# Kernel tuning notes

Measured on AMD Instinct MI355X. Metric: run time of the kernel, lower is better.

The kernel has to match this reference:

```python
import jax, jax.numpy as jnp
import numpy as np

C = 256

def setup_inputs() -> dict:
    key = jax.random.key(0)
    ks = jax.random.split(key, 9)
    B, H, W = 32, 32, 32
    s = C ** -0.5  # init scale for weights
    inputs = jax.random.normal(ks[0], (B, H, W, C), jnp.float32)
    Wq = jax.random.normal(ks[1], (C, C), jnp.float32) * s
    Wk = jax.random.normal(ks[2], (C, C), jnp.float32) * s
    Wv = jax.random.normal(ks[3], (C, C), jnp.float32) * s
    Wo = jax.random.normal(ks[4], (C, C), jnp.float32) * s
    bq = jnp.zeros((C,), jnp.float32)
    bk = jnp.zeros((C,), jnp.float32)
    bv = jnp.zeros((C,), jnp.float32)
    bo = jnp.zeros((C,), jnp.float32)
    return {"inputs": inputs, "Wq": Wq, "bq": bq, "Wk": Wk, "bk": bk,
            "Wv": Wv, "bv": bv, "Wo": Wo, "bo": bo}

def reference(inputs, Wq, bq, Wk, bk, Wv, bv, Wo, bo):
    B, H, W, c = inputs.shape
    scale = jnp.float32(c) ** -0.5
    x = inputs.reshape(B, H * W, c)           # 1x1 conv == per-pixel matmul
    q = x @ Wq + bq                           # [B, HW, C]
    k = x @ Wk + bk
    v = x @ Wv + bv
    scores = jnp.einsum('bnc,bmc->bnm', q, k) * scale  # [B, HW, HW]
    attn = jax.nn.softmax(scores, axis=-1)
    attended = jnp.einsum('bnm,bmc->bnc', attn, v)     # [B, HW, C]
    out = attended @ Wo + bo
    return out.reshape(B, H, W, c)
```

## Files before the change

### kernel.cpp

```cpp
#include <hip/hip_runtime.h>
#include <hip/hip_bf16.h>

typedef __bf16 bf16;
typedef __bf16 bf16x4 __attribute__((ext_vector_type(4)));
typedef __bf16 bf16x8 __attribute__((ext_vector_type(8)));
typedef float f32x4 __attribute__((ext_vector_type(4)));

#define SM_C 0.09016994374947424f

__global__ __launch_bounds__(256) void transpose_w(
    const float* __restrict__ Wq, const float* __restrict__ Wk,
    const float* __restrict__ Wv, const float* __restrict__ Wo,
    bf16* __restrict__ Wt)
{
    __shared__ float T[32][33];
    const int bid = blockIdx.x;
    const int m = bid >> 6, tile = bid & 63;
    const int tn0 = (tile >> 3) * 32, tk0 = (tile & 7) * 32;
    const float* W = (m == 0) ? Wq : (m == 1) ? Wk : (m == 2) ? Wv : Wo;

    const int t = threadIdx.x;
    const int r = t >> 3, c4 = (t & 7) * 4;

    f32x4 v = *(const f32x4*)(W + (size_t)(tk0 + r) * 256 + tn0 + c4);
#pragma unroll
    for (int j = 0; j < 4; ++j) T[r][c4 + j] = v[j];
    __syncthreads();

    bf16x4 ov;
#pragma unroll
    for (int j = 0; j < 4; ++j) ov[j] = (bf16)T[c4 + j][r];
    *(bf16x4*)(Wt + (size_t)m * 65536 + (size_t)(tn0 + r) * 256 + tk0 + c4) = ov;
}

__global__ __launch_bounds__(256, 3) void qkv_gemm(
    const float* __restrict__ X, const bf16* __restrict__ Wt,
    const float* __restrict__ bq, const float* __restrict__ bk,
    const float* __restrict__ bv,
    bf16* __restrict__ Qo, bf16* __restrict__ Ko, bf16* __restrict__ Vto)
{
    __shared__ __align__(16) char qsmem[36864];
    bf16* const Xs  = (bf16*)qsmem;
    bf16* const Ws_ = (bf16*)(qsmem + 18432);
    bf16* const Cs  = (bf16*)qsmem;

    const int t    = threadIdx.x;
    const int lane = t & 63, wv = t >> 6;
    const int quad = lane >> 4, l16 = lane & 15;
    const int bm   = blockIdx.x;
    const int bn   = blockIdx.y;
    const int proj = bn >> 1;

    const bf16* W = Wt + (size_t)proj * 65536 + (size_t)(bn & 1) * 32768;
    const float* bias = (proj == 0) ? bq : (proj == 1) ? bk : bv;

    const int m0 = t >> 3;
    const int c0 = (t & 7) * 8;

    const f32x4 zero = {0.0f, 0.0f, 0.0f, 0.0f};
    f32x4 acc[2][8];
#pragma unroll
    for (int i = 0; i < 2; ++i)
#pragma unroll
        for (int j = 0; j < 8; ++j) acc[i][j] = zero;

    f32x4 xa[4], xb[4]; bf16x8 wp[4];
#pragma unroll
    for (int p = 0; p < 4; ++p) {
        const float* px = X + (size_t)(bm * 128 + m0 + p * 32) * 256 + c0;
        xa[p] = *(const f32x4*)px; xb[p] = *(const f32x4*)(px + 4);
        wp[p] = *(const bf16x8*)(W + (size_t)(m0 + p * 32) * 256 + c0);
    }

    for (int kt = 0; kt < 4; ++kt) {
#pragma unroll
        for (int p = 0; p < 4; ++p) {
            bf16x8 r;
#pragma unroll
            for (int j = 0; j < 4; ++j) { r[j] = (bf16)xa[p][j]; r[j + 4] = (bf16)xb[p][j]; }
            *(bf16x8*)(Xs + (m0 + p * 32) * 72 + c0) = r;
            *(bf16x8*)(Ws_ + (m0 + p * 32) * 72 + c0) = wp[p];
        }
        __syncthreads();

        if (kt < 3) {
#pragma unroll
            for (int p = 0; p < 4; ++p) {
                const float* px = X + (size_t)(bm * 128 + m0 + p * 32) * 256 + (kt + 1) * 64 + c0;
                xa[p] = *(const f32x4*)px; xb[p] = *(const f32x4*)(px + 4);
                wp[p] = *(const bf16x8*)(W + (size_t)(m0 + p * 32) * 256 + (kt + 1) * 64 + c0);
            }
        }

#pragma unroll
        for (int ks = 0; ks < 2; ++ks) {
            bf16x8 a[2], bb[8];
#pragma unroll
            for (int mt = 0; mt < 2; ++mt)
                a[mt] = *(const bf16x8*)(Xs + (wv * 32 + mt * 16 + l16) * 72 + ks * 32 + quad * 8);
#pragma unroll
            for (int nt = 0; nt < 8; ++nt)
                bb[nt] = *(const bf16x8*)(Ws_ + (nt * 16 + l16) * 72 + ks * 32 + quad * 8);
#pragma unroll
            for (int mt = 0; mt < 2; ++mt)
#pragma unroll
                for (int nt = 0; nt < 8; ++nt)
                    acc[mt][nt] = __builtin_amdgcn_mfma_f32_16x16x32_bf16(
                        a[mt], bb[nt], acc[mt][nt], 0, 0, 0);
        }
        __syncthreads();
    }

    if (proj == 2) {
#pragma unroll
        for (int nt = 0; nt < 8; ++nt) {
            int col = (bn & 1) * 128 + nt * 16 + l16;
            float bvv = bias[col];
#pragma unroll
            for (int mt = 0; mt < 2; ++mt) {
                int grow0 = bm * 128 + wv * 32 + mt * 16 + quad * 4;
                bf16x4 pk;
#pragma unroll
                for (int r = 0; r < 4; ++r) pk[r] = (bf16)(acc[mt][nt][r] + bvv);
                int b = grow0 >> 10, m = grow0 & 1023;
                *(bf16x4*)(Vto + (size_t)b * 262144 + (size_t)col * 1024 + m) = pk;
            }
        }
    } else {
        bf16* dst = (proj == 0) ? Qo : Ko;
#pragma unroll
        for (int nt = 0; nt < 8; ++nt) {
            float bvv = bias[(bn & 1) * 128 + nt * 16 + l16];
#pragma unroll
            for (int mt = 0; mt < 2; ++mt)
#pragma unroll
                for (int r = 0; r < 4; ++r)
                    Cs[(wv * 32 + mt * 16 + quad * 4 + r) * 132 + nt * 16 + l16] =
                        (bf16)(acc[mt][nt][r] + bvv);
        }
        __syncthreads();
#pragma unroll
        for (int i = 0; i < 8; ++i) {
            int chunk = i * 256 + t;
            int row = chunk >> 4, cc = chunk & 15;
            bf16x8 v = *(const bf16x8*)(Cs + row * 132 + cc * 8);
            *(bf16x8*)(dst + (size_t)(bm * 128 + row) * 256 + (bn & 1) * 128 + cc * 8) = v;
        }
    }
}

__global__ __launch_bounds__(512, 2) void flash_attn(
    const bf16* __restrict__ Qr, const bf16* __restrict__ K,
    const bf16* __restrict__ Vt, const bf16* __restrict__ Wo,
    const float* __restrict__ bo, float* __restrict__ out)
{
    __shared__ __align__(16) char smem[142336];
    bf16* const Ksp0 = (bf16*)(smem);
    bf16* const Ksp1 = (bf16*)(smem + 16896);
    bf16* const Vsp0 = (bf16*)(smem + 33792);
    bf16* const Vsp1 = (bf16*)(smem + 54272);
    bf16* const Os   = (bf16*)(smem);
    bf16* const Wos  = (bf16*)(smem + 74752);

    const int t    = threadIdx.x;
    const int lane = t & 63, wv = t >> 6;
    const int quad = lane >> 4, l16 = lane & 15;
    const int b  = blockIdx.x;
    const int qt = blockIdx.y;

    char* const Pb = smem + 74752 + wv * 1024;

    bf16x8 qf[8];
    const size_t qrow = (size_t)b * 1024 + qt * 128 + wv * 16 + l16;
#pragma unroll
    for (int ks = 0; ks < 8; ++ks)
        qf[ks] = *(const bf16x8*)(Qr + qrow * 256 + ks * 32 + quad * 8);

    const f32x4 zero = {0.0f, 0.0f, 0.0f, 0.0f};
    f32x4 o[16];
#pragma unroll
    for (int n = 0; n < 16; ++n) o[n] = zero;
    float lst[4] = {0.f, 0.f, 0.f, 0.f};

    const int kv0 = t >> 4, kc0 = (t & 15) * 8;
    const int vc0 = t >> 1, vm0 = (t & 1) * 8;

    bf16x8 kp[2], vp[2];
#pragma unroll
    for (int p = 0; p < 2; ++p) {
        kp[p] = *(const bf16x8*)(K + (size_t)(b * 1024 + kv0) * 256 + kc0 + p * 128);
        vp[p] = *(const bf16x8*)(Vt + (size_t)b * 262144 + (size_t)vc0 * 1024 + vm0 + p * 16);
    }
#pragma unroll
    for (int p = 0; p < 2; ++p) {
        *(bf16x8*)(Ksp0 + kv0 * 264 + kc0 + p * 128) = kp[p];
        *(bf16x8*)(Vsp0 + vc0 * 40 + vm0 + p * 16) = vp[p];
    }
#pragma unroll
    for (int p = 0; p < 2; ++p) {
        kp[p] = *(const bf16x8*)(K + (size_t)(b * 1024 + 32 + kv0) * 256 + kc0 + p * 128);
        vp[p] = *(const bf16x8*)(Vt + (size_t)b * 262144 + (size_t)vc0 * 1024 + 32 + vm0 + p * 16);
    }

    for (int j = 0; j < 32; ++j) {
        const bf16* Kb = (j & 1) ? Ksp1 : Ksp0;
        const bf16* Vb = (j & 1) ? Vsp1 : Vsp0;
        __syncthreads();

        f32x4 s[2];
        s[0] = zero; s[1] = zero;
#pragma unroll
        for (int ks = 0; ks < 8; ++ks) {
#pragma unroll
            for (int n = 0; n < 2; ++n) {
                bf16x8 bfr = *(const bf16x8*)(Kb + (n * 16 + l16) * 264 + ks * 32 + quad * 8);
                s[n] = __builtin_amdgcn_mfma_f32_16x16x32_bf16(qf[ks], bfr, s[n], 0, 0, 0);
            }
        }

        if (j < 31) {
            bf16* Kn = (j & 1) ? Ksp0 : Ksp1;
            bf16* Vn = (j & 1) ? Vsp0 : Vsp1;
#pragma unroll
            for (int p = 0; p < 2; ++p) {
                *(bf16x8*)(Kn + kv0 * 264 + kc0 + p * 128) = kp[p];
                *(bf16x8*)(Vn + vc0 * 40 + vm0 + p * 16) = vp[p];
            }
            if (j < 30) {
#pragma unroll
                for (int p = 0; p < 2; ++p) {
                    kp[p] = *(const bf16x8*)(K + (size_t)(b * 1024 + (j + 2) * 32 + kv0) * 256 + kc0 + p * 128);
                    vp[p] = *(const bf16x8*)(Vt + (size_t)b * 262144 + (size_t)vc0 * 1024 + (j + 2) * 32 + vm0 + p * 16);
                }
            }
        }

#pragma unroll
        for (int n = 0; n < 2; ++n) {
#pragma unroll
            for (int r = 0; r < 4; ++r) {
                float pv = __builtin_amdgcn_exp2f(s[n][r] * SM_C);
                lst[r] += pv;
                int row = quad * 4 + r;
                *(bf16*)(Pb + ((row * 64 + n * 32 + l16 * 2) ^ ((row & 7) << 4))) = (bf16)pv;
            }
        }

        bf16x8 af = *(const bf16x8*)(Pb + ((l16 * 64 + quad * 16) ^ ((l16 & 7) << 4)));
#pragma unroll
        for (int n = 0; n < 16; ++n) {
            bf16x8 bfr = *(const bf16x8*)(Vb + (n * 16 + l16) * 40 + quad * 8);
            o[n] = __builtin_amdgcn_mfma_f32_16x16x32_bf16(af, bfr, o[n], 0, 0, 0);
        }
    }

    __syncthreads();

    float inv[4];
#pragma unroll
    for (int r = 0; r < 4; ++r) {
        float l = lst[r];
#pragma unroll
        for (int off = 1; off < 16; off <<= 1)
            l += __shfl_xor(l, off, 64);
        inv[r] = 1.0f / l;
    }
#pragma unroll
    for (int n = 0; n < 16; ++n)
#pragma unroll
        for (int r = 0; r < 4; ++r)
            Os[(wv * 16 + quad * 4 + r) * 264 + n * 16 + l16] = (bf16)(o[n][r] * inv[r]);

    const int rh = (wv & 1) * 64;
    const int nq = wv >> 1;
    const size_t orow0 = (size_t)b * 1024 + qt * 128 + rh;

#pragma unroll
    for (int h = 0; h < 2; ++h) {
        if (h) __syncthreads();
#pragma unroll
        for (int i = 0; i < 8; ++i) {
            int c = t + i * 512;
            int row = c >> 5, c8 = (c & 31) * 8;
            *(bf16x8*)(Wos + row * 264 + c8) =
                *(const bf16x8*)(Wo + (size_t)(h * 128 + row) * 256 + c8);
        }
        __syncthreads();

        f32x4 acc[4][2];
#pragma unroll
        for (int mt = 0; mt < 4; ++mt) { acc[mt][0] = zero; acc[mt][1] = zero; }

#pragma unroll
        for (int ks = 0; ks < 8; ++ks) {
            bf16x8 a[4], bb[2];
#pragma unroll
            for (int mt = 0; mt < 4; ++mt)
                a[mt] = *(const bf16x8*)(Os + (rh + mt * 16 + l16) * 264 + ks * 32 + quad * 8);
#pragma unroll
            for (int nt = 0; nt < 2; ++nt)
                bb[nt] = *(const bf16x8*)(Wos + (nq * 32 + nt * 16 + l16) * 264 + ks * 32 + quad * 8);
#pragma unroll
            for (int mt = 0; mt < 4; ++mt)
#pragma unroll
                for (int nt = 0; nt < 2; ++nt)
                    acc[mt][nt] = __builtin_amdgcn_mfma_f32_16x16x32_bf16(
                        a[mt], bb[nt], acc[mt][nt], 0, 0, 0);
        }

#pragma unroll
        for (int nt = 0; nt < 2; ++nt) {
            int col = h * 128 + nq * 32 + nt * 16 + l16;
            float bvv = bo[col];
#pragma unroll
            for (int mt = 0; mt < 4; ++mt) {
#pragma unroll
                for (int r = 0; r < 4; ++r) {
                    size_t row = orow0 + mt * 16 + quad * 4 + r;
                    out[row * 256 + col] = acc[mt][nt][r] + bvv;
                }
            }
        }
    }
}

extern "C" void kernel_launch(void* const* d_in, const int* in_sizes, int n_in,
                              void* d_out, int out_size, void* d_ws, size_t ws_size,
                              hipStream_t stream)
{
    (void)in_sizes; (void)n_in; (void)out_size; (void)ws_size;
    const float* X  = (const float*)d_in[0];
    const float* Wq = (const float*)d_in[1];
    const float* bq = (const float*)d_in[2];
    const float* Wk = (const float*)d_in[3];
    const float* bk = (const float*)d_in[4];
    const float* Wv = (const float*)d_in[5];
    const float* bv = (const float*)d_in[6];
    const float* Wo = (const float*)d_in[7];
    const float* bo = (const float*)d_in[8];
    float* out = (float*)d_out;

    const size_t NTOK = (size_t)32768 * 256;

    bf16* Wt  = (bf16*)d_ws;
    bf16* Qw  = (bf16*)d_ws + 262144;
    bf16* Kw  = Qw + NTOK;
    bf16* Vtw = Kw + NTOK;

    transpose_w<<<256, 256, 0, stream>>>(Wq, Wk, Wv, Wo, Wt);
    qkv_gemm   <<<dim3(256, 6), 256, 0, stream>>>(X, Wt, bq, bk, bv, Qw, Kw, Vtw);
    flash_attn <<<dim3(32, 8),  512, 0, stream>>>(Qw, Kw, Vtw, Wt + 3 * 65536, bo, out);
}
```

Baseline: 175.5 us.

## Restructure flash attention to 4 waves with direct global-to-LDS async loads

The attention kernel now runs 256 threads per block, and each wave handles 32 query rows (two 16-row tiles), so every K/V fragment read from LDS feeds twice as many MFMAs. K, V and Wo tiles are copied with global_load_lds straight into XOR-swizzled LDS buffers instead of being staged through registers. The output projection is split into eight 32-column slices. The aim is less register staging, fewer LDS bank conflicts and more reuse per LDS read. The cost is fewer waves per block to hide latency, more accumulator registers, and extra barriers in the Wo projection loop.

```diff
diff --git a/kernel.cpp b/kernel.cpp
--- a/kernel.cpp
+++ b/kernel.cpp
@@ -2,11 +2,15 @@
 #include <hip/hip_bf16.h>
 
 typedef __bf16 bf16;
+typedef __bf16 bf16x2 __attribute__((ext_vector_type(2)));
 typedef __bf16 bf16x4 __attribute__((ext_vector_type(4)));
 typedef __bf16 bf16x8 __attribute__((ext_vector_type(8)));
 typedef float f32x4 __attribute__((ext_vector_type(4)));
 
 #define SM_C 0.09016994374947424f
+
+typedef __attribute__((address_space(1))) const void as1_void;
+typedef __attribute__((address_space(3))) void as3_void;
 
 __global__ __launch_bounds__(256) void transpose_w(
     const float* __restrict__ Wq, const float* __restrict__ Wk,
@@ -149,18 +153,12 @@
     }
 }
 
-__global__ __launch_bounds__(512, 2) void flash_attn(
+__global__ __launch_bounds__(256, 2) void flash_attn(
     const bf16* __restrict__ Qr, const bf16* __restrict__ K,
     const bf16* __restrict__ Vt, const bf16* __restrict__ Wo,
     const float* __restrict__ bo, float* __restrict__ out)
 {
-    __shared__ __align__(16) char smem[142336];
-    bf16* const Ksp0 = (bf16*)(smem);
-    bf16* const Ksp1 = (bf16*)(smem + 16896);
-    bf16* const Vsp0 = (bf16*)(smem + 33792);
-    bf16* const Vsp1 = (bf16*)(smem + 54272);
-    bf16* const Os   = (bf16*)(smem);
-    bf16* const Wos  = (bf16*)(smem + 74752);
+    __shared__ __align__(16) char smem[81920];
 
     const int t    = threadIdx.x;
     const int lane = t & 63, wv = t >> 6;
@@ -168,158 +166,174 @@
     const int b  = blockIdx.x;
     const int qt = blockIdx.y;
 
-    char* const Pb = smem + 74752 + wv * 1024;
-
-    bf16x8 qf[8];
-    const size_t qrow = (size_t)b * 1024 + qt * 128 + wv * 16 + l16;
-#pragma unroll
-    for (int ks = 0; ks < 8; ++ks)
-        qf[ks] = *(const bf16x8*)(Qr + qrow * 256 + ks * 32 + quad * 8);
+    bf16x8 qf[2][8];
+#pragma unroll
+    for (int mt = 0; mt < 2; ++mt) {
+        const bf16* qp = Qr + ((size_t)b * 1024 + qt * 128 + wv * 32 + mt * 16 + l16) * 256 + quad * 8;
+#pragma unroll
+        for (int ks = 0; ks < 8; ++ks)
+            qf[mt][ks] = *(const bf16x8*)(qp + ks * 32);
+    }
 
     const f32x4 zero = {0.0f, 0.0f, 0.0f, 0.0f};
-    f32x4 o[16];
-#pragma unroll
-    for (int n = 0; n < 16; ++n) o[n] = zero;
-    float lst[4] = {0.f, 0.f, 0.f, 0.f};
-
-    const int kv0 = t >> 4, kc0 = (t & 15) * 8;
-    const int vc0 = t >> 1, vm0 = (t & 1) * 8;
-
-    bf16x8 kp[2], vp[2];
-#pragma unroll
-    for (int p = 0; p < 2; ++p) {
-        kp[p] = *(const bf16x8*)(K + (size_t)(b * 1024 + kv0) * 256 + kc0 + p * 128);
-        vp[p] = *(const bf16x8*)(Vt + (size_t)b * 262144 + (size_t)vc0 * 1024 + vm0 + p * 16);
-    }
-#pragma unroll
-    for (int p = 0; p < 2; ++p) {
-        *(bf16x8*)(Ksp0 + kv0 * 264 + kc0 + p * 128) = kp[p];
-        *(bf16x8*)(Vsp0 + vc0 * 40 + vm0 + p * 16) = vp[p];
-    }
-#pragma unroll
-    for (int p = 0; p < 2; ++p) {
-        kp[p] = *(const bf16x8*)(K + (size_t)(b * 1024 + 32 + kv0) * 256 + kc0 + p * 128);
-        vp[p] = *(const bf16x8*)(Vt + (size_t)b * 262144 + (size_t)vc0 * 1024 + 32 + vm0 + p * 16);
-    }
+    f32x4 o[2][16];
+#pragma unroll
+    for (int mt = 0; mt < 2; ++mt)
+#pragma unroll
+        for (int n = 0; n < 16; ++n) o[mt][n] = zero;
+    float lst[2] = {0.f, 0.f};
+
+    auto gloadK = [&](int T, int buf) {
+#pragma unroll
+        for (int p = 0; p < 4; ++p) {
+            int chunk = wv * 4 + p;
+            int row   = chunk * 2 + (lane >> 5);
+            int s     = (lane & 31) ^ (row & 7);
+            const bf16* gsrc = K + ((size_t)b * 1024 + T * 32 + row) * 256 + s * 8;
+            __builtin_amdgcn_global_load_lds((as1_void*)gsrc,
+                (as3_void*)(smem + buf * 16384 + chunk * 1024), 16, 0, 0);
+        }
+    };
+    auto gloadV = [&](int T, int buf) {
+#pragma unroll
+        for (int p = 0; p < 4; ++p) {
+            int chunk = wv * 4 + p;
+            int row   = chunk * 16 + (lane >> 2);
+            int s     = (lane & 3) ^ (row & 3);
+            const bf16* gsrc = Vt + (size_t)b * 262144 + (size_t)row * 1024 + T * 32 + s * 8;
+            __builtin_amdgcn_global_load_lds((as1_void*)gsrc,
+                (as3_void*)(smem + 32768 + buf * 16384 + chunk * 1024), 16, 0, 0);
+        }
+    };
+
+    char* const Pb = smem + 65536 + wv * 1024;
+    const int psw = (l16 & 7) << 4;
+
+    gloadK(0, 0); gloadV(0, 0);
 
     for (int j = 0; j < 32; ++j) {
-        const bf16* Kb = (j & 1) ? Ksp1 : Ksp0;
-        const bf16* Vb = (j & 1) ? Vsp1 : Vsp0;
-        __syncthreads();
-
-        f32x4 s[2];
-        s[0] = zero; s[1] = zero;
+        const int buf = j & 1;
+        __syncthreads();
+
+        if (j < 31) { gloadK(j + 1, buf ^ 1); gloadV(j + 1, buf ^ 1); }
+
+        f32x4 s2[2][2];
+        s2[0][0] = zero; s2[0][1] = zero; s2[1][0] = zero; s2[1][1] = zero;
+        const char* Kb = smem + buf * 16384;
 #pragma unroll
         for (int ks = 0; ks < 8; ++ks) {
 #pragma unroll
             for (int n = 0; n < 2; ++n) {
-                bf16x8 bfr = *(const bf16x8*)(Kb + (n * 16 + l16) * 264 + ks * 32 + quad * 8);
-                s[n] = __builtin_amdgcn_mfma_f32_16x16x32_bf16(qf[ks], bfr, s[n], 0, 0, 0);
-            }
-        }
-
-        if (j < 31) {
-            bf16* Kn = (j & 1) ? Ksp0 : Ksp1;
-            bf16* Vn = (j & 1) ? Vsp0 : Vsp1;
-#pragma unroll
-            for (int p = 0; p < 2; ++p) {
-                *(bf16x8*)(Kn + kv0 * 264 + kc0 + p * 128) = kp[p];
-                *(bf16x8*)(Vn + vc0 * 40 + vm0 + p * 16) = vp[p];
-            }
-            if (j < 30) {
-#pragma unroll
-                for (int p = 0; p < 2; ++p) {
-                    kp[p] = *(const bf16x8*)(K + (size_t)(b * 1024 + (j + 2) * 32 + kv0) * 256 + kc0 + p * 128);
-                    vp[p] = *(const bf16x8*)(Vt + (size_t)b * 262144 + (size_t)vc0 * 1024 + (j + 2) * 32 + vm0 + p * 16);
+                bf16x8 kb = *(const bf16x8*)(Kb + (n * 16 + l16) * 512 +
+                                             (((ks * 4 + quad) ^ (l16 & 7)) << 4));
+                s2[0][n] = __builtin_amdgcn_mfma_f32_16x16x32_bf16(kb, qf[0][ks], s2[0][n], 0, 0, 0);
+                s2[1][n] = __builtin_amdgcn_mfma_f32_16x16x32_bf16(kb, qf[1][ks], s2[1][n], 0, 0, 0);
+            }
+        }
+
+        bf16x8 af[2];
+#pragma unroll
+        for (int mt = 0; mt < 2; ++mt) {
+#pragma unroll
+            for (int n = 0; n < 2; ++n) {
+#pragma unroll
+                for (int h = 0; h < 2; ++h) {
+                    float p0 = __builtin_amdgcn_exp2f(s2[mt][n][2 * h] * SM_C);
+                    float p1 = __builtin_amdgcn_exp2f(s2[mt][n][2 * h + 1] * SM_C);
+                    lst[mt] += p0 + p1;
+                    bf16x2 pk; pk[0] = (bf16)p0; pk[1] = (bf16)p1;
+                    *(bf16x2*)(Pb + ((l16 * 64 + n * 32 + quad * 8 + h * 4) ^ psw)) = pk;
                 }
             }
-        }
-
-#pragma unroll
-        for (int n = 0; n < 2; ++n) {
+            af[mt] = *(const bf16x8*)(Pb + ((l16 * 64 + quad * 16) ^ psw));
+        }
+
+        const char* Vb = smem + 32768 + buf * 16384;
+#pragma unroll
+        for (int n = 0; n < 16; ++n) {
+            bf16x8 vb = *(const bf16x8*)(Vb + (n * 16 + l16) * 64 +
+                                         ((quad ^ (l16 & 3)) << 4));
+            o[0][n] = __builtin_amdgcn_mfma_f32_16x16x32_bf16(af[0], vb, o[0][n], 0, 0, 0);
+            o[1][n] = __builtin_amdgcn_mfma_f32_16x16x32_bf16(af[1], vb, o[1][n], 0, 0, 0);
+        }
+    }
+
+    __syncthreads();
+
+#pragma unroll
+    for (int mt = 0; mt < 2; ++mt) {
+        lst[mt] += __shfl_xor(lst[mt], 16, 64);
+        lst[mt] += __shfl_xor(lst[mt], 32, 64);
+    }
+    float inv[2][4];
+#pragma unroll
+    for (int mt = 0; mt < 2; ++mt)
+#pragma unroll
+        for (int r = 0; r < 4; ++r)
+            inv[mt][r] = 1.0f / __shfl(lst[mt], quad * 4 + r, 64);
+
+#pragma unroll
+    for (int mt = 0; mt < 2; ++mt)
+#pragma unroll
+        for (int n = 0; n < 16; ++n)
 #pragma unroll
             for (int r = 0; r < 4; ++r) {
-                float pv = __builtin_amdgcn_exp2f(s[n][r] * SM_C);
-                lst[r] += pv;
-                int row = quad * 4 + r;
-                *(bf16*)(Pb + ((row * 64 + n * 32 + l16 * 2) ^ ((row & 7) << 4))) = (bf16)pv;
-            }
-        }
-
-        bf16x8 af = *(const bf16x8*)(Pb + ((l16 * 64 + quad * 16) ^ ((l16 & 7) << 4)));
-#pragma unroll
-        for (int n = 0; n < 16; ++n) {
-            bf16x8 bfr = *(const bf16x8*)(Vb + (n * 16 + l16) * 40 + quad * 8);
-            o[n] = __builtin_amdgcn_mfma_f32_16x16x32_bf16(af, bfr, o[n], 0, 0, 0);
-        }
-    }
-
-    __syncthreads();
-
-    float inv[4];
-#pragma unroll
-    for (int r = 0; r < 4; ++r) {
-        float l = lst[r];
-#pragma unroll
-        for (int off = 1; off < 16; off <<= 1)
-            l += __shfl_xor(l, off, 64);
-        inv[r] = 1.0f / l;
-    }
-#pragma unroll
-    for (int n = 0; n < 16; ++n)
-#pragma unroll
-        for (int r = 0; r < 4; ++r)
-            Os[(wv * 16 + quad * 4 + r) * 264 + n * 16 + l16] = (bf16)(o[n][r] * inv[r]);
-
-    const int rh = (wv & 1) * 64;
-    const int nq = wv >> 1;
-    const size_t orow0 = (size_t)b * 1024 + qt * 128 + rh;
-
-#pragma unroll
-    for (int h = 0; h < 2; ++h) {
-        if (h) __syncthreads();
-#pragma unroll
-        for (int i = 0; i < 8; ++i) {
-            int c = t + i * 512;
-            int row = c >> 5, c8 = (c & 31) * 8;
-            *(bf16x8*)(Wos + row * 264 + c8) =
-                *(const bf16x8*)(Wo + (size_t)(h * 128 + row) * 256 + c8);
-        }
-        __syncthreads();
-
-        f32x4 acc[4][2];
-#pragma unroll
-        for (int mt = 0; mt < 4; ++mt) { acc[mt][0] = zero; acc[mt][1] = zero; }
-
+                int row = wv * 32 + mt * 16 + quad * 4 + r;
+                int col = n * 16 + l16;
+                *(bf16*)(smem + row * 512 + ((col * 2) ^ ((row & 7) << 4))) =
+                    (bf16)(o[mt][n][r] * inv[mt][r]);
+            }
+
+    const size_t orow0 = (size_t)b * 1024 + qt * 128 + wv * 32;
+    for (int sl = 0; sl < 8; ++sl) {
+        __syncthreads();
+#pragma unroll
+        for (int p = 0; p < 4; ++p) {
+            int chunk = wv * 4 + p;
+            int row   = chunk * 2 + (lane >> 5);
+            int s     = (lane & 31) ^ (row & 7);
+            const bf16* gsrc = Wo + (size_t)(sl * 32 + row) * 256 + s * 8;
+            __builtin_amdgcn_global_load_lds((as1_void*)gsrc,
+                (as3_void*)(smem + 65536 + chunk * 1024), 16, 0, 0);
+        }
+        __syncthreads();
+
+        f32x4 acc[2][2];
+        acc[0][0] = zero; acc[0][1] = zero; acc[1][0] = zero; acc[1][1] = zero;
 #pragma unroll
         for (int ks = 0; ks < 8; ++ks) {
-            bf16x8 a[4], bb[2];
-#pragma unroll
-            for (int mt = 0; mt < 4; ++mt)
-                a[mt] = *(const bf16x8*)(Os + (rh + mt * 16 + l16) * 264 + ks * 32 + quad * 8);
-#pragma unroll
-            for (int nt = 0; nt < 2; ++nt)
-                bb[nt] = *(const bf16x8*)(Wos + (nq * 32 + nt * 16 + l16) * 264 + ks * 32 + quad * 8);
-#pragma unroll
-            for (int mt = 0; mt < 4; ++mt)
-#pragma unroll
-                for (int nt = 0; nt < 2; ++nt)
-                    acc[mt][nt] = __builtin_amdgcn_mfma_f32_16x16x32_bf16(
-                        a[mt], bb[nt], acc[mt][nt], 0, 0, 0);
-        }
-
-#pragma unroll
-        for (int nt = 0; nt < 2; ++nt) {
-            int col = h * 128 + nq * 32 + nt * 16 + l16;
+            bf16x8 a[2], bb[2];
+#pragma unroll
+            for (int rt = 0; rt < 2; ++rt) {
+                int row = wv * 32 + rt * 16 + l16;
+                a[rt] = *(const bf16x8*)(smem + row * 512 +
+                                         (((ks * 4 + quad) ^ (l16 & 7)) << 4));
+            }
+#pragma unroll
+            for (int ct = 0; ct < 2; ++ct) {
+                int row = ct * 16 + l16;
+                bb[ct] = *(const bf16x8*)(smem + 65536 + row * 512 +
+                                          (((ks * 4 + quad) ^ (l16 & 7)) << 4));
+            }
+#pragma unroll
+            for (int rt = 0; rt < 2; ++rt)
+#pragma unroll
+                for (int ct = 0; ct < 2; ++ct)
+                    acc[rt][ct] = __builtin_amdgcn_mfma_f32_16x16x32_bf16(
+                        a[rt], bb[ct], acc[rt][ct], 0, 0, 0);
+        }
+
+#pragma unroll
+        for (int ct = 0; ct < 2; ++ct) {
+            int col = sl * 32 + ct * 16 + l16;
             float bvv = bo[col];
 #pragma unroll
-            for (int mt = 0; mt < 4; ++mt) {
+            for (int rt = 0; rt < 2; ++rt)
 #pragma unroll
                 for (int r = 0; r < 4; ++r) {
-                    size_t row = orow0 + mt * 16 + quad * 4 + r;
-                    out[row * 256 + col] = acc[mt][nt][r] + bvv;
+                    size_t row = orow0 + rt * 16 + quad * 4 + r;
+                    out[row * 256 + col] = acc[rt][ct][r] + bvv;
                 }
-            }
         }
     }
 }
@@ -349,5 +363,5 @@
 
     transpose_w<<<256, 256, 0, stream>>>(Wq, Wk, Wv, Wo, Wt);
     qkv_gemm   <<<dim3(256, 6), 256, 0, stream>>>(X, Wt, bq, bk, bv, Qw, Kw, Vtw);
-    flash_attn <<<dim3(32, 8),  512, 0, stream>>>(Qw, Kw, Vtw, Wt + 3 * 65536, bo, out);
+    flash_attn <<<dim3(32, 8),  256, 0, stream>>>(Qw, Kw, Vtw, Wt + 3 * 65536, bo, out);
 }
```

Result: slower. 187.3 us (+6.7%).

## Compute transposed scores in attention and stage V-transpose stores through LDS

Applied to the files above, without the earlier changes.

In the attention loop the QK^T MFMA now takes K as the A operand and Q as the B operand, which yields transposed scores. Each lane then holds consecutive kv positions for one query row, so exp values are packed into bf16x2 LDS stores, and the row-sum becomes one scalar per lane reduced by two cross-quad shuffles. Separately, the V projection epilogue writes its tile into shared memory and emits coalesced 16-byte stores of the transposed V, replacing scattered 8-byte global writes. This adds an extra syncthreads and LDS pass in the GEMM epilogue.

```diff
diff --git a/kernel.cpp b/kernel.cpp
--- a/kernel.cpp
+++ b/kernel.cpp
@@ -2,6 +2,7 @@
 #include <hip/hip_bf16.h>
 
 typedef __bf16 bf16;
+typedef __bf16 bf16x2 __attribute__((ext_vector_type(2)));
 typedef __bf16 bf16x4 __attribute__((ext_vector_type(4)));
 typedef __bf16 bf16x8 __attribute__((ext_vector_type(8)));
 typedef float f32x4 __attribute__((ext_vector_type(4)));
@@ -43,6 +44,7 @@
     bf16* const Xs  = (bf16*)qsmem;
     bf16* const Ws_ = (bf16*)(qsmem + 18432);
     bf16* const Cs  = (bf16*)qsmem;
+    bf16* const Cs2 = (bf16*)qsmem;
 
     const int t    = threadIdx.x;
     const int lane = t & 63, wv = t >> 6;
@@ -114,17 +116,26 @@
     if (proj == 2) {
 #pragma unroll
         for (int nt = 0; nt < 8; ++nt) {
-            int col = (bn & 1) * 128 + nt * 16 + l16;
-            float bvv = bias[col];
+            int cl = nt * 16 + l16;
+            float bvv = bias[(bn & 1) * 128 + cl];
 #pragma unroll
             for (int mt = 0; mt < 2; ++mt) {
-                int grow0 = bm * 128 + wv * 32 + mt * 16 + quad * 4;
+                int r0 = wv * 32 + mt * 16 + quad * 4;
                 bf16x4 pk;
 #pragma unroll
                 for (int r = 0; r < 4; ++r) pk[r] = (bf16)(acc[mt][nt][r] + bvv);
-                int b = grow0 >> 10, m = grow0 & 1023;
-                *(bf16x4*)(Vto + (size_t)b * 262144 + (size_t)col * 1024 + m) = pk;
-            }
+                *(bf16x4*)(Cs2 + cl * 136 + r0) = pk;
+            }
+        }
+        __syncthreads();
+        const int bq = bm >> 3, moff = (bm & 7) * 128;
+#pragma unroll
+        for (int i = 0; i < 8; ++i) {
+            int chunk = i * 256 + t;
+            int cl = chunk >> 4, rp = (chunk & 15) * 8;
+            bf16x8 v = *(const bf16x8*)(Cs2 + cl * 136 + rp);
+            *(bf16x8*)(Vto + (size_t)bq * 262144 +
+                       (size_t)((bn & 1) * 128 + cl) * 1024 + moff + rp) = v;
         }
     } else {
         bf16* dst = (proj == 0) ? Qo : Ko;
@@ -169,6 +180,7 @@
     const int qt = blockIdx.y;
 
     char* const Pb = smem + 74752 + wv * 1024;
+    const int psw = (l16 & 7) << 4;
 
     bf16x8 qf[8];
     const size_t qrow = (size_t)b * 1024 + qt * 128 + wv * 16 + l16;
@@ -180,7 +192,7 @@
     f32x4 o[16];
 #pragma unroll
     for (int n = 0; n < 16; ++n) o[n] = zero;
-    float lst[4] = {0.f, 0.f, 0.f, 0.f};
+    float lst = 0.f;
 
     const int kv0 = t >> 4, kc0 = (t & 15) * 8;
     const int vc0 = t >> 1, vm0 = (t & 1) * 8;
@@ -212,9 +224,9 @@
 #pragma unroll
         for (int ks = 0; ks < 8; ++ks) {
 #pragma unroll
-            for (int n = 0; n < 2; ++n) {
-                bf16x8 bfr = *(const bf16x8*)(Kb + (n * 16 + l16) * 264 + ks * 32 + quad * 8);
-                s[n] = __builtin_amdgcn_mfma_f32_16x16x32_bf16(qf[ks], bfr, s[n], 0, 0, 0);
+            for (int kvt = 0; kvt < 2; ++kvt) {
+                bf16x8 kb = *(const bf16x8*)(Kb + (kvt * 16 + l16) * 264 + ks * 32 + quad * 8);
+                s[kvt] = __builtin_amdgcn_mfma_f32_16x16x32_bf16(kb, qf[ks], s[kvt], 0, 0, 0);
             }
         }
 
@@ -236,17 +248,18 @@
         }
 
 #pragma unroll
-        for (int n = 0; n < 2; ++n) {
-#pragma unroll
-            for (int r = 0; r < 4; ++r) {
-                float pv = __builtin_amdgcn_exp2f(s[n][r] * SM_C);
-                lst[r] += pv;
-                int row = quad * 4 + r;
-                *(bf16*)(Pb + ((row * 64 + n * 32 + l16 * 2) ^ ((row & 7) << 4))) = (bf16)pv;
-            }
-        }
-
-        bf16x8 af = *(const bf16x8*)(Pb + ((l16 * 64 + quad * 16) ^ ((l16 & 7) << 4)));
+        for (int kvt = 0; kvt < 2; ++kvt) {
+#pragma unroll
+            for (int h = 0; h < 2; ++h) {
+                float p0 = __builtin_amdgcn_exp2f(s[kvt][2 * h] * SM_C);
+                float p1 = __builtin_amdgcn_exp2f(s[kvt][2 * h + 1] * SM_C);
+                lst += p0 + p1;
+                bf16x2 pk; pk[0] = (bf16)p0; pk[1] = (bf16)p1;
+                *(bf16x2*)(Pb + ((l16 * 64 + kvt * 32 + quad * 8 + h * 4) ^ psw)) = pk;
+            }
+        }
+
+        bf16x8 af = *(const bf16x8*)(Pb + ((l16 * 64 + quad * 16) ^ psw));
 #pragma unroll
         for (int n = 0; n < 16; ++n) {
             bf16x8 bfr = *(const bf16x8*)(Vb + (n * 16 + l16) * 40 + quad * 8);
@@ -256,15 +269,13 @@
 
     __syncthreads();
 
+    lst += __shfl_xor(lst, 16, 64);
+    lst += __shfl_xor(lst, 32, 64);
     float inv[4];
 #pragma unroll
-    for (int r = 0; r < 4; ++r) {
-        float l = lst[r];
-#pragma unroll
-        for (int off = 1; off < 16; off <<= 1)
-            l += __shfl_xor(l, off, 64);
-        inv[r] = 1.0f / l;
-    }
+    for (int r = 0; r < 4; ++r)
+        inv[r] = 1.0f / __shfl(lst, quad * 4 + r, 64);
+
 #pragma unroll
     for (int n = 0; n < 16; ++n)
 #pragma unroll
@@ -349,5 +360,5 @@
 
     transpose_w<<<256, 256, 0, stream>>>(Wq, Wk, Wv, Wo, Wt);
     qkv_gemm   <<<dim3(256, 6), 256, 0, stream>>>(X, Wt, bq, bk, bv, Qw, Kw, Vtw);
-    flash_attn <<<dim3(32, 8),  512, 0, stream>>>(Qw, Kw, Vtw, Wt + 3 * 65536, bo, out);
+    flash_attn <<<dim3(32, 8), 512, 0, stream>>>(Qw, Kw, Vtw, Wt + 3 * 65536, bo, out);
 }
```

Measured after the change: 171.7 us. 2.2% less time.
